# Kernel optimization log

Hardware: AMD Instinct MI355X
Metric: run time of the kernel (lower is better)

## Reference

```python
import jax, jax.numpy as jnp
import numpy as np


def setup_inputs() -> dict:
    key = jax.random.key(0)
    kq, kk, kv, kl = jax.random.split(key, 4)
    B, H, S, D = 2, 8, 1024, 64
    Q = jax.random.normal(kq, (B, H, S, D), dtype=jnp.float32)
    K = jax.random.normal(kk, (B, H, S, D), dtype=jnp.float32)
    V = jax.random.normal(kv, (B, H, S, D), dtype=jnp.float32)
    valid_lens = jax.random.randint(kl, (B, S), 0, S, dtype=jnp.int64)
    return {"Q": Q, "K": K, "V": V, "valid_lens": valid_lens}


def reference(Q, K, V, valid_lens):
    # Q,K,V: [B,H,S,D]. The torch repeat/reshape makes K[b,i,j]=K[b,j],
    # i.e. every query head i attends to every key/value head j.
    B, H, S, D = Q.shape
    inv_sqrt = 1.0 / jnp.sqrt(jnp.asarray(D, dtype=Q.dtype))
    # score[b,i,j,s,t] = Q[b,i,s,:] . K[b,j,t,:] / sqrt(D)
    score = jnp.einsum('bisd,bjtd->bijst', Q, K) * inv_sqrt
    attention_weights = jax.nn.softmax(score, axis=-1)  # [B,H,H,S,S]
    # ctx[b,i,s,d] = sum_j sum_t w[b,i,j,s,t] * V[b,j,t,d]  (matmul then sum over j)
    ctx = jnp.einsum('bijst,bjtd->bisd', attention_weights, V)  # [B,H,S,D]
    context = jnp.transpose(ctx, (0, 2, 1, 3)).reshape(B, S, H * D)  # [B,S,H*D]
    return context, attention_weights
```

## Files before the change

kernel.cpp:

```cpp
#include <hip/hip_runtime.h>
#include <hip/hip_bf16.h>

#define B_ 2
#define H_ 8
#define S_ 1024
#define D_ 64
#define PLP 264
#define STRIP (16 * PLP)

typedef short short8 __attribute__((ext_vector_type(8)));
typedef float f32x4 __attribute__((ext_vector_type(4)));

__device__ __forceinline__ unsigned int f2bf(float f) {
  union { float f; unsigned int u; } v; v.f = f;
  return (v.u + 0x7fffu + ((v.u >> 16) & 1u)) >> 16;
}
__device__ __forceinline__ float bf2f(unsigned int bits) {
  union { unsigned int u; float f; } v; v.u = bits << 16;
  return v.f;
}
__device__ __forceinline__ unsigned int cvt_pk_bf16(float lo, float hi) {
  unsigned int r;
  asm("v_cvt_pk_bf16_f32 %0, %1, %2" : "=v"(r) : "v"(lo), "v"(hi));
  return r;
}

__global__ void conv_bf16_kernel(const float* __restrict__ src,
                                 unsigned short* __restrict__ dst, int n4) {
  int idx = blockIdx.x * blockDim.x + threadIdx.x;
  if (idx >= n4) return;
  const float4 v = ((const float4*)src)[idx];
  unsigned int lo = f2bf(v.x) | (f2bf(v.y) << 16);
  unsigned int hi = f2bf(v.z) | (f2bf(v.w) << 16);
  ((uint2*)dst)[idx] = make_uint2(lo, hi);
}

__global__ void transpose_v_kernel(const float* __restrict__ V,
                                   unsigned short* __restrict__ Vt) {
  __shared__ float tile[64][65];
  int bh = blockIdx.x >> 4;
  int t0 = (blockIdx.x & 15) * 64;
  int tid = threadIdx.x;
  int cx = tid & 63, ry = tid >> 6;
  const float* src = V + ((size_t)bh * S_ + t0) * D_;
#pragma unroll
  for (int r = 0; r < 16; ++r) {
    int row = r * 4 + ry;
    tile[row][cx] = src[(size_t)row * D_ + cx];
  }
  __syncthreads();
  unsigned short* dst = Vt + (size_t)bh * D_ * S_ + t0;
#pragma unroll
  for (int r = 0; r < 16; ++r) {
    int d = r * 4 + ry;
    dst[(size_t)d * S_ + cx] = (unsigned short)f2bf(tile[cx][d]);
  }
}

__global__ __launch_bounds__(256, 2) void attn_kernel(
    const unsigned short* __restrict__ Qb,
    const unsigned short* __restrict__ Kb,
    const unsigned short* __restrict__ Vt,
    float* __restrict__ w_out,
    float* __restrict__ ctx_out)
{
  const int tid  = threadIdx.x;
  const int w    = tid >> 6;
  const int lane = tid & 63;
  const int g = lane >> 4;
  const int c = lane & 15;
  const int raw = blockIdx.x;
  const int bid = (raw & 7) * 64 + (raw >> 3);
  const int sb = bid & 31;
  const int i  = (bid >> 5) & 7;
  const int b  = bid >> 8;
  const int s0 = sb * 32;
  const int t0 = w * 256;

  __shared__ __align__(16) unsigned short pstrips[8 * STRIP];
  __shared__ float ssum[2][4][32];
  unsigned short* stripA = pstrips + (2 * w) * STRIP;
  unsigned short* stripB = stripA + STRIP;

  const unsigned short* qrowA =
      Qb + ((size_t)((b * H_ + i) * S_) + s0 + c) * D_ + g * 8;
  short8 qa0 = *(const short8*)(qrowA);
  short8 qa1 = *(const short8*)(qrowA + 32);
  const unsigned short* qrowB = qrowA + 16 * D_;
  short8 qb0 = *(const short8*)(qrowB);
  short8 qb1 = *(const short8*)(qrowB + 32);

  f32x4 ctxA[4], ctxB[4];
#pragma unroll
  for (int nt = 0; nt < 4; ++nt) {
    ctxA[nt] = (f32x4){0.f, 0.f, 0.f, 0.f};
    ctxB[nt] = (f32x4){0.f, 0.f, 0.f, 0.f};
  }

  const float SC = 0.18033688011112042f;

  for (int j = 0; j < H_; ++j) {
    const int par = j & 1;
    const unsigned short* kbase = Kb + (size_t)((b * H_ + j) * S_) * D_;

    float rsA = 0.f, rsB = 0.f;
#pragma unroll
    for (int tt = 0; tt < 16; ++tt) {
      const unsigned short* kr = kbase + (size_t)(t0 + tt * 16 + c) * D_ + g * 8;
      short8 kf0 = *(const short8*)(kr);
      short8 kf1 = *(const short8*)(kr + 32);
      f32x4 accA = (f32x4){0.f, 0.f, 0.f, 0.f};
      accA = __builtin_amdgcn_mfma_f32_16x16x32_bf16(kf0, qa0, accA, 0, 0, 0);
      accA = __builtin_amdgcn_mfma_f32_16x16x32_bf16(kf1, qa1, accA, 0, 0, 0);
      f32x4 accB = (f32x4){0.f, 0.f, 0.f, 0.f};
      accB = __builtin_amdgcn_mfma_f32_16x16x32_bf16(kf0, qb0, accB, 0, 0, 0);
      accB = __builtin_amdgcn_mfma_f32_16x16x32_bf16(kf1, qb1, accB, 0, 0, 0);
      float a0 = exp2f(accA[0] * SC);
      float a1 = exp2f(accA[1] * SC);
      float a2 = exp2f(accA[2] * SC);
      float a3 = exp2f(accA[3] * SC);
      rsA += (a0 + a1) + (a2 + a3);
      uint2 pkA = make_uint2(cvt_pk_bf16(a0, a1), cvt_pk_bf16(a2, a3));
      *(uint2*)&stripA[c * PLP + tt * 16 + 4 * g] = pkA;
      float b0 = exp2f(accB[0] * SC);
      float b1 = exp2f(accB[1] * SC);
      float b2 = exp2f(accB[2] * SC);
      float b3 = exp2f(accB[3] * SC);
      rsB += (b0 + b1) + (b2 + b3);
      uint2 pkB = make_uint2(cvt_pk_bf16(b0, b1), cvt_pk_bf16(b2, b3));
      *(uint2*)&stripB[c * PLP + tt * 16 + 4 * g] = pkB;
    }
    rsA += __shfl_xor(rsA, 16, 64);
    rsA += __shfl_xor(rsA, 32, 64);
    rsB += __shfl_xor(rsB, 16, 64);
    rsB += __shfl_xor(rsB, 32, 64);
    if (lane < 16) {
      ssum[par][w][lane] = rsA;
      ssum[par][w][16 + lane] = rsB;
    }

    f32x4 pvA[4], pvB[4];
#pragma unroll
    for (int nt = 0; nt < 4; ++nt) {
      pvA[nt] = (f32x4){0.f, 0.f, 0.f, 0.f};
      pvB[nt] = (f32x4){0.f, 0.f, 0.f, 0.f};
    }
    const unsigned short* vbase =
        Vt + ((size_t)((b * H_ + j) * D_) + c) * S_ + t0 + g * 8;
#pragma unroll
    for (int ch = 0; ch < 8; ++ch) {
      short8 paA = *(const short8*)&stripA[c * PLP + ch * 32 + g * 8];
      short8 paB = *(const short8*)&stripB[c * PLP + ch * 32 + g * 8];
#pragma unroll
      for (int nt = 0; nt < 4; ++nt) {
        short8 vf = *(const short8*)(vbase + (size_t)nt * 16 * S_ + ch * 32);
        pvA[nt] = __builtin_amdgcn_mfma_f32_16x16x32_bf16(paA, vf, pvA[nt], 0, 0, 0);
        pvB[nt] = __builtin_amdgcn_mfma_f32_16x16x32_bf16(paB, vf, pvB[nt], 0, 0, 0);
      }
    }

    asm volatile("s_waitcnt lgkmcnt(0)\n\ts_barrier" ::: "memory");

    float fsA = ssum[par][0][c] + ssum[par][1][c] + ssum[par][2][c] + ssum[par][3][c];
    float fsB = ssum[par][0][16 + c] + ssum[par][1][16 + c] +
                ssum[par][2][16 + c] + ssum[par][3][16 + c];
    float iqA = 1.f / fsA;
    float iqB = 1.f / fsB;

    {
      float ar0 = __shfl(iqA, 4 * g + 0, 64);
      float ar1 = __shfl(iqA, 4 * g + 1, 64);
      float ar2 = __shfl(iqA, 4 * g + 2, 64);
      float ar3 = __shfl(iqA, 4 * g + 3, 64);
      float br0 = __shfl(iqB, 4 * g + 0, 64);
      float br1 = __shfl(iqB, 4 * g + 1, 64);
      float br2 = __shfl(iqB, 4 * g + 2, 64);
      float br3 = __shfl(iqB, 4 * g + 3, 64);
#pragma unroll
      for (int nt = 0; nt < 4; ++nt) {
        ctxA[nt][0] += pvA[nt][0] * ar0;
        ctxA[nt][1] += pvA[nt][1] * ar1;
        ctxA[nt][2] += pvA[nt][2] * ar2;
        ctxA[nt][3] += pvA[nt][3] * ar3;
        ctxB[nt][0] += pvB[nt][0] * br0;
        ctxB[nt][1] += pvB[nt][1] * br1;
        ctxB[nt][2] += pvB[nt][2] * br2;
        ctxB[nt][3] += pvB[nt][3] * br3;
      }
    }

    float* wbase = w_out +
        ((size_t)((b * H_ + i) * H_ + j) * S_ + s0) * S_ + t0 + lane * 4;
#pragma unroll
    for (int r = 0; r < 16; ++r) {
      const float iq =
          __uint_as_float(__builtin_amdgcn_readlane(__float_as_uint(iqA), r));
      uint2 pv2 = *(const uint2*)&stripA[r * PLP + lane * 4];
      f32x4 ww;
      ww[0] = bf2f(pv2.x & 0xffffu) * iq;
      ww[1] = bf2f(pv2.x >> 16)     * iq;
      ww[2] = bf2f(pv2.y & 0xffffu) * iq;
      ww[3] = bf2f(pv2.y >> 16)     * iq;
      __builtin_nontemporal_store(ww, (f32x4*)(wbase + (size_t)r * S_));
    }
#pragma unroll
    for (int r = 0; r < 16; ++r) {
      const float iq =
          __uint_as_float(__builtin_amdgcn_readlane(__float_as_uint(iqB), r));
      uint2 pv2 = *(const uint2*)&stripB[r * PLP + lane * 4];
      f32x4 ww;
      ww[0] = bf2f(pv2.x & 0xffffu) * iq;
      ww[1] = bf2f(pv2.x >> 16)     * iq;
      ww[2] = bf2f(pv2.y & 0xffffu) * iq;
      ww[3] = bf2f(pv2.y >> 16)     * iq;
      __builtin_nontemporal_store(ww, (f32x4*)(wbase + (size_t)(16 + r) * S_));
    }
  }

  __syncthreads();
  float (*ctile)[32][68] = (float(*)[32][68])pstrips;
#pragma unroll
  for (int nt = 0; nt < 4; ++nt)
#pragma unroll
    for (int r = 0; r < 4; ++r) {
      ctile[w][4 * g + r][nt * 16 + c] = ctxA[nt][r];
      ctile[w][16 + 4 * g + r][nt * 16 + c] = ctxB[nt][r];
    }
  __syncthreads();
#pragma unroll
  for (int it = 0; it < 2; ++it) {
    const int slot = it * 256 + tid;
    const int r  = slot >> 4;
    const int d0 = (slot & 15) * 4;
    f32x4 a0 = *(const f32x4*)&ctile[0][r][d0];
    f32x4 a1 = *(const f32x4*)&ctile[1][r][d0];
    f32x4 a2 = *(const f32x4*)&ctile[2][r][d0];
    f32x4 a3 = *(const f32x4*)&ctile[3][r][d0];
    f32x4 s = a0 + a1 + a2 + a3;
    *(f32x4*)(ctx_out + ((size_t)(b * S_ + s0 + r) * (H_ * D_) + i * D_ + d0)) = s;
  }
}

extern "C" void kernel_launch(void* const* d_in, const int* in_sizes, int n_in,
                              void* d_out, int out_size, void* d_ws, size_t ws_size,
                              hipStream_t stream) {
  const float* Q = (const float*)d_in[0];
  const float* K = (const float*)d_in[1];
  const float* V = (const float*)d_in[2];

  const size_t nelem = (size_t)B_ * H_ * S_ * D_;
  float* outc = (float*)d_out;
  float* outw = outc + (size_t)B_ * S_ * H_ * D_;

  unsigned short* Qb = (unsigned short*)d_ws;
  unsigned short* Kb = Qb + nelem;
  unsigned short* Vt = Kb + nelem;

  conv_bf16_kernel<<<1024, 256, 0, stream>>>(Q, Qb, (int)(nelem / 4));
  conv_bf16_kernel<<<1024, 256, 0, stream>>>(K, Kb, (int)(nelem / 4));
  transpose_v_kernel<<<256, 256, 0, stream>>>(V, Vt);

  attn_kernel<<<B_ * H_ * (S_ / 32), 256, 0, stream>>>(Qb, Kb, Vt, outw, outc);
}
```

Before: 161.7 us.

## Prefetch next head's K tiles into registers and stagger head order

Register-prefetches the first half of the next key head's K fragments before the attention-weight store loop, so those loads overlap the large nontemporal writes. Also rotates the j loop start by query-head parity, so blocks with different i start on different K heads and spread cache and memory traffic. A sched_barrier keeps the prefetch ahead of the stores. The cost is 16 extra short8 registers per lane, which may lower occupancy or cause spills.

```diff
diff --git a/kernel.cpp b/kernel.cpp
--- a/kernel.cpp
+++ b/kernel.cpp
@@ -76,6 +76,7 @@
   const int b  = bid >> 8;
   const int s0 = sb * 32;
   const int t0 = w * 256;
+  const int phase = (i & 1) * 4;
 
   __shared__ __align__(16) unsigned short pstrips[8 * STRIP];
   __shared__ float ssum[2][4][32];
@@ -99,16 +100,40 @@
 
   const float SC = 0.18033688011112042f;
 
-  for (int j = 0; j < H_; ++j) {
-    const int par = j & 1;
+  short8 kpre[16];
+#define PREFETCH_K(jidx)                                                      \
+  {                                                                           \
+    const unsigned short* kb2 =                                               \
+        Kb + (size_t)((b * H_ + (jidx)) * S_) * D_;                           \
+    _Pragma("unroll")                                                         \
+    for (int tt = 0; tt < 8; ++tt) {                                          \
+      const unsigned short* kr =                                              \
+          kb2 + (size_t)(t0 + tt * 16 + c) * D_ + g * 8;                      \
+      kpre[2 * tt]     = *(const short8*)(kr);                                \
+      kpre[2 * tt + 1] = *(const short8*)(kr + 32);                           \
+    }                                                                         \
+  }
+
+  PREFETCH_K(phase);
+
+  for (int jj = 0; jj < H_; ++jj) {
+    const int j   = (jj + phase) & 7;
+    const int par = jj & 1;
     const unsigned short* kbase = Kb + (size_t)((b * H_ + j) * S_) * D_;
 
     float rsA = 0.f, rsB = 0.f;
 #pragma unroll
     for (int tt = 0; tt < 16; ++tt) {
-      const unsigned short* kr = kbase + (size_t)(t0 + tt * 16 + c) * D_ + g * 8;
-      short8 kf0 = *(const short8*)(kr);
-      short8 kf1 = *(const short8*)(kr + 32);
+      short8 kf0, kf1;
+      if (tt < 8) {
+        kf0 = kpre[2 * tt];
+        kf1 = kpre[2 * tt + 1];
+      } else {
+        const unsigned short* kr =
+            kbase + (size_t)(t0 + tt * 16 + c) * D_ + g * 8;
+        kf0 = *(const short8*)(kr);
+        kf1 = *(const short8*)(kr + 32);
+      }
       f32x4 accA = (f32x4){0.f, 0.f, 0.f, 0.f};
       accA = __builtin_amdgcn_mfma_f32_16x16x32_bf16(kf0, qa0, accA, 0, 0, 0);
       accA = __builtin_amdgcn_mfma_f32_16x16x32_bf16(kf1, qa1, accA, 0, 0, 0);
@@ -189,6 +214,12 @@
       }
     }
 
+    if (jj < H_ - 1) {
+      const int jn = (jj + 1 + phase) & 7;
+      PREFETCH_K(jn);
+    }
+    __builtin_amdgcn_sched_barrier(0);
+
     float* wbase = w_out +
         ((size_t)((b * H_ + i) * H_ + j) * S_ + s0) * S_ + t0 + lane * 4;
 #pragma unroll
@@ -216,6 +247,7 @@
       __builtin_nontemporal_store(ww, (f32x4*)(wbase + (size_t)(16 + r) * S_));
     }
   }
+#undef PREFETCH_K
 
   __syncthreads();
   float (*ctile)[32][68] = (float(*)[32][68])pstrips;
```

After: 165.8 us. 1.03x slower.
